# Performance work log

Hardware: AMD Instinct MI355X
Metric: run time of the kernel (lower is better)

## Reference

```python
import jax, jax.numpy as jnp
import numpy as np

H, F, E, K = 1024, 4096, 8, 2
B, S = 2, 2048

def setup_inputs() -> dict:
    key = jax.random.key(0)
    ks = jax.random.split(key, 5)
    scale = 0.02
    return {
        "x": jax.random.normal(ks[0], (B, S, H), dtype=jnp.float32),
        "router_w": jax.random.normal(ks[1], (H, E), dtype=jnp.float32) * scale,
        "router_b": jnp.zeros((E,), dtype=jnp.float32),
        "w1": jax.random.normal(ks[2], (E, H, F), dtype=jnp.float32) * scale,
        "b1": jnp.zeros((E, F), dtype=jnp.float32),
        "w2": jax.random.normal(ks[3], (E, F, H), dtype=jnp.float32) * scale,
        "b2": jnp.zeros((E, H), dtype=jnp.float32),
        "k": K,
    }

def reference(x, router_w, router_b, w1, b1, w2, b2, k):
    # Router: softmax over experts, then top-k
    scores = jnp.einsum('bsh,he->bse', x, router_w) + router_b          # [B,S,E]
    probs = jax.nn.softmax(scores, axis=-1)
    p, expert_id = jax.lax.top_k(probs, k)                               # [B,S,k]
    # Dense all-expert MLP (math identical to per-expert gather/scatter)
    h = jax.nn.gelu(jnp.einsum('bsh,ehf->bsef', x, w1) + b1,
                    approximate=False)                                    # [B,S,E,F]
    out_all = jnp.einsum('bsef,efh->bseh', h, w2) + b2                    # [B,S,E,H]
    # Gather the k selected experts per token
    out = jnp.take_along_axis(out_all, expert_id[..., None], axis=2)     # [B,S,k,H]
    # Normalize top-k probs and combine
    p = p / jnp.sum(p, axis=-1, keepdims=True)                            # [B,S,k]
    return jnp.sum(p[..., None] * out, axis=2)                            # [B,S,H]
```

## Files before the change

kernel.cpp:

```cpp
#include <hip/hip_runtime.h>
#include <hip/hip_bf16.h>
#include <math.h>

#define H 1024
#define F 4096
#define E 8
#define NTOK 4096
#define CAP 4096
#define NPAIR 8192

typedef unsigned short u16;
typedef __bf16 bf16x8 __attribute__((ext_vector_type(8)));
typedef float f32x4 __attribute__((ext_vector_type(4)));
typedef u16 u16x8 __attribute__((ext_vector_type(8)));
typedef u16 u16x4 __attribute__((ext_vector_type(4)));

__device__ inline u16 f2bf(float f) {
    union { float f; unsigned u; } v; v.f = f;
    unsigned r = v.u + 0x7fffu + ((v.u >> 16) & 1u);
    return (u16)(r >> 16);
}

__device__ inline void gload_lds16(const void* g, void* l) {
    __builtin_amdgcn_global_load_lds(
        (const __attribute__((address_space(1))) unsigned*)g,
        (__attribute__((address_space(3))) unsigned*)l, 16, 0, 0);
}

__global__ void cvt_x(const float* __restrict__ x, u16* __restrict__ xb, int n8) {
    int j = blockIdx.x * blockDim.x + threadIdx.x;
    if (j >= n8) return;
    const float4* p = (const float4*)(x + (size_t)j * 8);
    float4 a = p[0], b = p[1];
    u16x8 o;
    o[0] = f2bf(a.x); o[1] = f2bf(a.y); o[2] = f2bf(a.z); o[3] = f2bf(a.w);
    o[4] = f2bf(b.x); o[5] = f2bf(b.y); o[6] = f2bf(b.z); o[7] = f2bf(b.w);
    *(u16x8*)(xb + (size_t)j * 8) = o;
}

__global__ void transpose_cvt(const float* __restrict__ in, u16* __restrict__ out,
                              int R, int C) {
    const float* ip = in + (size_t)blockIdx.z * R * C;
    u16* op = out + (size_t)blockIdx.z * R * C;
    __shared__ float tile[64][65];
    int r0 = blockIdx.y * 64, c0 = blockIdx.x * 64;
    int tid = threadIdx.x;
    int rr = tid >> 4;
    int cc4 = (tid & 15) * 4;
    #pragma unroll
    for (int it = 0; it < 4; ++it) {
        int r = rr + it * 16;
        float4 v = *(const float4*)&ip[(size_t)(r0 + r) * C + c0 + cc4];
        tile[r][cc4 + 0] = v.x; tile[r][cc4 + 1] = v.y;
        tile[r][cc4 + 2] = v.z; tile[r][cc4 + 3] = v.w;
    }
    __syncthreads();
    int co = tid >> 3;
    int ro8 = (tid & 7) * 8;
    #pragma unroll
    for (int it = 0; it < 2; ++it) {
        int c = co + it * 32;
        u16x8 o;
        #pragma unroll
        for (int u = 0; u < 8; ++u) o[u] = f2bf(tile[ro8 + u][c]);
        *(u16x8*)&op[(size_t)(c0 + c) * R + r0 + ro8] = o;
    }
}

__global__ void router_kernel(const float* __restrict__ x, const float* __restrict__ rw,
                              const float* __restrict__ rb, int* __restrict__ counts,
                              int* __restrict__ tok_e, float* __restrict__ wgt_e) {
    int tok = blockIdx.x;
    int lane = threadIdx.x;
    float s[E] = {0.f,0.f,0.f,0.f,0.f,0.f,0.f,0.f};
    for (int r = 0; r < 4; ++r) {
        int h = r * 256 + lane * 4;
        float4 xv = *(const float4*)&x[(size_t)tok * H + h];
        const float* xf = (const float*)&xv;
        #pragma unroll
        for (int u = 0; u < 4; ++u) {
            float xs = xf[u];
            const float4* row = (const float4*)&rw[(size_t)(h + u) * E];
            float4 a = row[0], b = row[1];
            s[0] += xs * a.x; s[1] += xs * a.y; s[2] += xs * a.z; s[3] += xs * a.w;
            s[4] += xs * b.x; s[5] += xs * b.y; s[6] += xs * b.z; s[7] += xs * b.w;
        }
    }
    #pragma unroll
    for (int off = 32; off > 0; off >>= 1)
        #pragma unroll
        for (int e2 = 0; e2 < E; ++e2) s[e2] += __shfl_down(s[e2], off);
    if (lane == 0) {
        #pragma unroll
        for (int e2 = 0; e2 < E; ++e2) s[e2] += rb[e2];
        int i0 = 0;
        #pragma unroll
        for (int e2 = 1; e2 < E; ++e2) if (s[e2] > s[i0]) i0 = e2;
        int i1 = (i0 == 0) ? 1 : 0;
        #pragma unroll
        for (int e2 = 0; e2 < E; ++e2) if (e2 != i0 && s[e2] > s[i1]) i1 = e2;
        float p0 = 1.0f / (1.0f + expf(s[i1] - s[i0]));
        float p1 = 1.0f - p0;
        int pos0 = atomicAdd(&counts[i0], 1);
        tok_e[i0 * CAP + pos0] = tok; wgt_e[i0 * CAP + pos0] = p0;
        int pos1 = atomicAdd(&counts[i1], 1);
        tok_e[i1 * CAP + pos1] = tok; wgt_e[i1 * CAP + pos1] = p1;
    }
}

__global__ void scan_kernel(const int* __restrict__ counts, int* __restrict__ offsets) {
    if (threadIdx.x == 0 && blockIdx.x == 0) {
        int acc = 0;
        for (int e2 = 0; e2 < E; ++e2) { offsets[e2] = acc; acc += counts[e2]; }
    }
}

#define BM 128
#define BN 128
#define BK 32

__global__ void gemm1_kernel(const u16* __restrict__ xb, const u16* __restrict__ w1t,
                             const float* __restrict__ b1,
                             const int* __restrict__ counts, const int* __restrict__ offsets,
                             const int* __restrict__ tok_e, u16* __restrict__ hbuf) {
    int e = blockIdx.z;
    int rows = counts[e];
    int m0 = blockIdx.y * BM;
    if (m0 >= rows) return;
    int n0 = blockIdx.x * BN;
    int off = offsets[e];
    const u16* wB = w1t + (size_t)e * F * H;

    __shared__ u16 As[BM * BK];
    __shared__ u16 Bs[BN * BK];

    int tid = threadIdx.x, lane = tid & 63, w = tid >> 6;
    int wr = w >> 1, wc = w & 1;

    int i0 = w * 2, i1 = w * 2 + 1;
    int rA0 = i0 * 16 + (lane >> 2), rA1 = i1 * 16 + (lane >> 2);
    int cB = (lane & 3) * 8;
    int ia0 = m0 + rA0; if (ia0 >= rows) ia0 = rows - 1;
    int ia1 = m0 + rA1; if (ia1 >= rows) ia1 = rows - 1;
    const u16* aS0 = xb + (size_t)tok_e[e * CAP + ia0] * H + cB;
    const u16* aS1 = xb + (size_t)tok_e[e * CAP + ia1] * H + cB;
    const u16* bS0 = wB + (size_t)(n0 + rA0) * H + cB;
    const u16* bS1 = wB + (size_t)(n0 + rA1) * H + cB;
    u16* lA0 = As + i0 * 512;  u16* lA1 = As + i1 * 512;
    u16* lB0 = Bs + i0 * 512;  u16* lB1 = Bs + i1 * 512;

    int fr = lane & 15, fk = (lane >> 4) * 8;
    const u16* pa = As + (wr * 64 + fr) * BK + fk;
    const u16* pb = Bs + (wc * 64 + fr) * BK + fk;

    f32x4 acc[4][4] = {};

    for (int k0 = 0; k0 < H; k0 += BK) {
        __syncthreads();
        gload_lds16(aS0 + k0, lA0);
        gload_lds16(aS1 + k0, lA1);
        gload_lds16(bS0 + k0, lB0);
        gload_lds16(bS1 + k0, lB1);
        __syncthreads();
        bf16x8 af[4], bfr[4];
        #pragma unroll
        for (int m = 0; m < 4; ++m) af[m] = *(const bf16x8*)(pa + m * 16 * BK);
        #pragma unroll
        for (int n = 0; n < 4; ++n) bfr[n] = *(const bf16x8*)(pb + n * 16 * BK);
        #pragma unroll
        for (int m = 0; m < 4; ++m)
            #pragma unroll
            for (int n = 0; n < 4; ++n)
                acc[m][n] = __builtin_amdgcn_mfma_f32_16x16x32_bf16(bfr[n], af[m], acc[m][n], 0, 0, 0);
    }

    const float* b1e = b1 + (size_t)e * F;
    int c4 = (lane >> 4) * 4;
    #pragma unroll
    for (int m = 0; m < 4; ++m) {
        int r = m0 + wr * 64 + m * 16 + fr;
        if (r < rows) {
            u16* hrow = hbuf + (size_t)(off + r) * F;
            #pragma unroll
            for (int n = 0; n < 4; ++n) {
                int gc = n0 + wc * 64 + n * 16 + c4;
                float4 bv = *(const float4*)&b1e[gc];
                const float* bvf = (const float*)&bv;
                u16x4 ov;
                #pragma unroll
                for (int j = 0; j < 4; ++j) {
                    float v = acc[m][n][j] + bvf[j];
                    float g = 0.5f * v * (1.0f + erff(v * 0.70710678118654752f));
                    ov[j] = f2bf(g);
                }
                *(u16x4*)&hrow[gc] = ov;
            }
        }
    }
}

__global__ void gemm2_kernel(const u16* __restrict__ hbuf, const u16* __restrict__ w2t,
                             const float* __restrict__ b2,
                             const int* __restrict__ counts, const int* __restrict__ offsets,
                             const int* __restrict__ tok_e, const float* __restrict__ wgt_e,
                             float* __restrict__ out) {
    int e = blockIdx.z;
    int rows = counts[e];
    int m0 = blockIdx.y * BM;
    if (m0 >= rows) return;
    int n0 = blockIdx.x * BN;
    int off = offsets[e];
    const u16* wB = w2t + (size_t)e * H * F;

    __shared__ u16 As[BM * BK];
    __shared__ u16 Bs[BN * BK];

    int tid = threadIdx.x, lane = tid & 63, w = tid >> 6;
    int wr = w >> 1, wc = w & 1;

    int i0 = w * 2, i1 = w * 2 + 1;
    int rA0 = i0 * 16 + (lane >> 2), rA1 = i1 * 16 + (lane >> 2);
    int cB = (lane & 3) * 8;
    int ia0 = m0 + rA0; if (ia0 >= rows) ia0 = rows - 1;
    int ia1 = m0 + rA1; if (ia1 >= rows) ia1 = rows - 1;
    const u16* aS0 = hbuf + (size_t)(off + ia0) * F + cB;
    const u16* aS1 = hbuf + (size_t)(off + ia1) * F + cB;
    const u16* bS0 = wB + (size_t)(n0 + rA0) * F + cB;
    const u16* bS1 = wB + (size_t)(n0 + rA1) * F + cB;
    u16* lA0 = As + i0 * 512;  u16* lA1 = As + i1 * 512;
    u16* lB0 = Bs + i0 * 512;  u16* lB1 = Bs + i1 * 512;

    int fr = lane & 15, fk = (lane >> 4) * 8;
    const u16* pa = As + (wr * 64 + fr) * BK + fk;
    const u16* pb = Bs + (wc * 64 + fr) * BK + fk;

    f32x4 acc[4][4] = {};

    for (int k0 = 0; k0 < F; k0 += BK) {
        __syncthreads();
        gload_lds16(aS0 + k0, lA0);
        gload_lds16(aS1 + k0, lA1);
        gload_lds16(bS0 + k0, lB0);
        gload_lds16(bS1 + k0, lB1);
        __syncthreads();
        bf16x8 af[4], bfr[4];
        #pragma unroll
        for (int m = 0; m < 4; ++m) af[m] = *(const bf16x8*)(pa + m * 16 * BK);
        #pragma unroll
        for (int n = 0; n < 4; ++n) bfr[n] = *(const bf16x8*)(pb + n * 16 * BK);
        #pragma unroll
        for (int m = 0; m < 4; ++m)
            #pragma unroll
            for (int n = 0; n < 4; ++n)
                acc[m][n] = __builtin_amdgcn_mfma_f32_16x16x32_bf16(bfr[n], af[m], acc[m][n], 0, 0, 0);
    }

    const float* b2e = b2 + (size_t)e * H;
    int c4 = (lane >> 4) * 4;
    #pragma unroll
    for (int m = 0; m < 4; ++m) {
        int r = m0 + wr * 64 + m * 16 + fr;
        if (r < rows) {
            int tok = tok_e[e * CAP + r];
            float wgt = wgt_e[e * CAP + r];
            float* orow = out + (size_t)tok * H;
            #pragma unroll
            for (int n = 0; n < 4; ++n) {
                int gc = n0 + wc * 64 + n * 16 + c4;
                float4 bv = *(const float4*)&b2e[gc];
                const float* bvf = (const float*)&bv;
                #pragma unroll
                for (int j = 0; j < 4; ++j)
                    atomicAdd(&orow[gc + j], (acc[m][n][j] + bvf[j]) * wgt);
            }
        }
    }
}

extern "C" void kernel_launch(void* const* d_in, const int* in_sizes, int n_in,
                              void* d_out, int out_size, void* d_ws, size_t ws_size,
                              hipStream_t stream) {
    const float* x  = (const float*)d_in[0];
    const float* rw = (const float*)d_in[1];
    const float* rb = (const float*)d_in[2];
    const float* w1 = (const float*)d_in[3];
    const float* b1 = (const float*)d_in[4];
    const float* w2 = (const float*)d_in[5];
    const float* b2 = (const float*)d_in[6];
    float* out = (float*)d_out;

    char* ws = (char*)d_ws;
    size_t o = 0;
    u16* xb   = (u16*)(ws + o); o += (size_t)NTOK * H * 2;
    u16* w1t  = (u16*)(ws + o); o += (size_t)E * F * H * 2;
    u16* w2t  = (u16*)(ws + o); o += (size_t)E * H * F * 2;
    u16* hbuf = (u16*)(ws + o); o += (size_t)NPAIR * F * 2;
    int*   tok_e = (int*)(ws + o);   o += (size_t)E * CAP * 4;
    float* wgt_e = (float*)(ws + o); o += (size_t)E * CAP * 4;
    int*   counts  = (int*)(ws + o); o += E * 4;
    int*   offsets = (int*)(ws + o); o += E * 4;

    hipMemsetAsync(counts, 0, 2 * E * sizeof(int), stream);
    hipMemsetAsync(out, 0, (size_t)out_size * sizeof(float), stream);

    cvt_x<<<(NTOK * H / 8 + 255) / 256, 256, 0, stream>>>(x, xb, NTOK * H / 8);
    transpose_cvt<<<dim3(F / 64, H / 64, E), 256, 0, stream>>>(w1, w1t, H, F);
    transpose_cvt<<<dim3(H / 64, F / 64, E), 256, 0, stream>>>(w2, w2t, F, H);
    router_kernel<<<NTOK, 64, 0, stream>>>(x, rw, rb, counts, tok_e, wgt_e);
    scan_kernel<<<1, 64, 0, stream>>>(counts, offsets);
    gemm1_kernel<<<dim3(F / BN, CAP / BM, E), 256, 0, stream>>>(xb, w1t, b1, counts, offsets, tok_e, hbuf);
    gemm2_kernel<<<dim3(H / BN, CAP / BM, E), 256, 0, stream>>>(hbuf, w2t, b2, counts, offsets, tok_e, wgt_e, out);
}
```

Baseline: 776.2 us.

## Triple-buffer GEMM LDS loads and replace atomic scatter with a combine kernel

Both expert GEMMs now use a three-stage LDS ring with async global-to-LDS loads issued two tiles ahead and a single barrier per k-step gated by vmcnt. This hides global load latency behind MFMA work and drops one barrier per iteration. GEMM2 no longer does float atomicAdd scatter into the output. It writes per-pair results to a dense fp32 buffer, and a new combine kernel gathers each token's two rows, adds the bias and applies the weights. The cost is an extra 32MB buffer written and read back, plus one more launch, in exchange for removing the atomics and the output memset.

```diff
diff --git a/kernel.cpp b/kernel.cpp
--- a/kernel.cpp
+++ b/kernel.cpp
@@ -69,7 +69,8 @@
 
 __global__ void router_kernel(const float* __restrict__ x, const float* __restrict__ rw,
                               const float* __restrict__ rb, int* __restrict__ counts,
-                              int* __restrict__ tok_e, float* __restrict__ wgt_e) {
+                              int* __restrict__ tok_e,
+                              int* __restrict__ pair_id, float* __restrict__ pair_w) {
     int tok = blockIdx.x;
     int lane = threadIdx.x;
     float s[E] = {0.f,0.f,0.f,0.f,0.f,0.f,0.f,0.f};
@@ -102,9 +103,11 @@
         float p0 = 1.0f / (1.0f + expf(s[i1] - s[i0]));
         float p1 = 1.0f - p0;
         int pos0 = atomicAdd(&counts[i0], 1);
-        tok_e[i0 * CAP + pos0] = tok; wgt_e[i0 * CAP + pos0] = p0;
+        tok_e[i0 * CAP + pos0] = tok;
         int pos1 = atomicAdd(&counts[i1], 1);
-        tok_e[i1 * CAP + pos1] = tok; wgt_e[i1 * CAP + pos1] = p1;
+        tok_e[i1 * CAP + pos1] = tok;
+        pair_id[tok * 2]     = i0 * CAP + pos0;  pair_w[tok * 2]     = p0;
+        pair_id[tok * 2 + 1] = i1 * CAP + pos1;  pair_w[tok * 2 + 1] = p1;
     }
 }
 
@@ -118,11 +121,13 @@
 #define BM 128
 #define BN 128
 #define BK 32
-
-__global__ void gemm1_kernel(const u16* __restrict__ xb, const u16* __restrict__ w1t,
-                             const float* __restrict__ b1,
-                             const int* __restrict__ counts, const int* __restrict__ offsets,
-                             const int* __restrict__ tok_e, u16* __restrict__ hbuf) {
+#define NBUF 3
+
+__global__ __launch_bounds__(256, 3)
+void gemm1_kernel(const u16* __restrict__ xb, const u16* __restrict__ w1t,
+                  const float* __restrict__ b1,
+                  const int* __restrict__ counts, const int* __restrict__ offsets,
+                  const int* __restrict__ tok_e, u16* __restrict__ hbuf) {
     int e = blockIdx.z;
     int rows = counts[e];
     int m0 = blockIdx.y * BM;
@@ -131,13 +136,13 @@
     int off = offsets[e];
     const u16* wB = w1t + (size_t)e * F * H;
 
-    __shared__ u16 As[BM * BK];
-    __shared__ u16 Bs[BN * BK];
+    __shared__ u16 As[NBUF][BM * BK];
+    __shared__ u16 Bs[NBUF][BN * BK];
 
     int tid = threadIdx.x, lane = tid & 63, w = tid >> 6;
     int wr = w >> 1, wc = w & 1;
 
-    int i0 = w * 2, i1 = w * 2 + 1;
+    int i0 = w * 2, i1 = i0 + 1;
     int rA0 = i0 * 16 + (lane >> 2), rA1 = i1 * 16 + (lane >> 2);
     int cB = (lane & 3) * 8;
     int ia0 = m0 + rA0; if (ia0 >= rows) ia0 = rows - 1;
@@ -146,27 +151,53 @@
     const u16* aS1 = xb + (size_t)tok_e[e * CAP + ia1] * H + cB;
     const u16* bS0 = wB + (size_t)(n0 + rA0) * H + cB;
     const u16* bS1 = wB + (size_t)(n0 + rA1) * H + cB;
-    u16* lA0 = As + i0 * 512;  u16* lA1 = As + i1 * 512;
-    u16* lB0 = Bs + i0 * 512;  u16* lB1 = Bs + i1 * 512;
+    int lc0 = i0 * 512, lc1 = i1 * 512;
 
     int fr = lane & 15, fk = (lane >> 4) * 8;
-    const u16* pa = As + (wr * 64 + fr) * BK + fk;
-    const u16* pb = Bs + (wc * 64 + fr) * BK + fk;
+    int aoff = (wr * 64 + fr) * BK + fk;
+    int boff = (wc * 64 + fr) * BK + fk;
 
     f32x4 acc[4][4] = {};
-
-    for (int k0 = 0; k0 < H; k0 += BK) {
-        __syncthreads();
-        gload_lds16(aS0 + k0, lA0);
-        gload_lds16(aS1 + k0, lA1);
-        gload_lds16(bS0 + k0, lB0);
-        gload_lds16(bS1 + k0, lB1);
-        __syncthreads();
+    const int NT = H / BK;
+
+    #define STAGE1(t, b) do { int kk = (t) * BK;                 \
+        gload_lds16(aS0 + kk, &As[b][lc0]);                      \
+        gload_lds16(aS1 + kk, &As[b][lc1]);                      \
+        gload_lds16(bS0 + kk, &Bs[b][lc0]);                      \
+        gload_lds16(bS1 + kk, &Bs[b][lc1]); } while (0)
+
+    STAGE1(0, 0);
+    STAGE1(1, 1);
+    int b = 0;
+    for (int t = 0; t < NT - 1; ++t) {
+        asm volatile("s_waitcnt vmcnt(4)" ::: "memory");
+        __builtin_amdgcn_s_barrier();
+        __builtin_amdgcn_sched_barrier(0);
+        if (t + 2 < NT) {
+            int bn = b + 2; if (bn >= NBUF) bn -= NBUF;
+            STAGE1(t + 2, bn);
+        }
         bf16x8 af[4], bfr[4];
         #pragma unroll
-        for (int m = 0; m < 4; ++m) af[m] = *(const bf16x8*)(pa + m * 16 * BK);
-        #pragma unroll
-        for (int n = 0; n < 4; ++n) bfr[n] = *(const bf16x8*)(pb + n * 16 * BK);
+        for (int m = 0; m < 4; ++m) af[m] = *(const bf16x8*)&As[b][aoff + m * 16 * BK];
+        #pragma unroll
+        for (int n = 0; n < 4; ++n) bfr[n] = *(const bf16x8*)&Bs[b][boff + n * 16 * BK];
+        #pragma unroll
+        for (int m = 0; m < 4; ++m)
+            #pragma unroll
+            for (int n = 0; n < 4; ++n)
+                acc[m][n] = __builtin_amdgcn_mfma_f32_16x16x32_bf16(bfr[n], af[m], acc[m][n], 0, 0, 0);
+        ++b; if (b >= NBUF) b -= NBUF;
+    }
+    asm volatile("s_waitcnt vmcnt(0)" ::: "memory");
+    __builtin_amdgcn_s_barrier();
+    __builtin_amdgcn_sched_barrier(0);
+    {
+        bf16x8 af[4], bfr[4];
+        #pragma unroll
+        for (int m = 0; m < 4; ++m) af[m] = *(const bf16x8*)&As[b][aoff + m * 16 * BK];
+        #pragma unroll
+        for (int n = 0; n < 4; ++n) bfr[n] = *(const bf16x8*)&Bs[b][boff + n * 16 * BK];
         #pragma unroll
         for (int m = 0; m < 4; ++m)
             #pragma unroll
@@ -199,11 +230,10 @@
     }
 }
 
-__global__ void gemm2_kernel(const u16* __restrict__ hbuf, const u16* __restrict__ w2t,
-                             const float* __restrict__ b2,
-                             const int* __restrict__ counts, const int* __restrict__ offsets,
-                             const int* __restrict__ tok_e, const float* __restrict__ wgt_e,
-                             float* __restrict__ out) {
+__global__ __launch_bounds__(256, 3)
+void gemm2_kernel(const u16* __restrict__ hbuf, const u16* __restrict__ w2t,
+                  const int* __restrict__ counts, const int* __restrict__ offsets,
+                  float* __restrict__ obuf) {
     int e = blockIdx.z;
     int rows = counts[e];
     int m0 = blockIdx.y * BM;
@@ -212,13 +242,13 @@
     int off = offsets[e];
     const u16* wB = w2t + (size_t)e * H * F;
 
-    __shared__ u16 As[BM * BK];
-    __shared__ u16 Bs[BN * BK];
+    __shared__ u16 As[NBUF][BM * BK];
+    __shared__ u16 Bs[NBUF][BN * BK];
 
     int tid = threadIdx.x, lane = tid & 63, w = tid >> 6;
     int wr = w >> 1, wc = w & 1;
 
-    int i0 = w * 2, i1 = w * 2 + 1;
+    int i0 = w * 2, i1 = i0 + 1;
     int rA0 = i0 * 16 + (lane >> 2), rA1 = i1 * 16 + (lane >> 2);
     int cB = (lane & 3) * 8;
     int ia0 = m0 + rA0; if (ia0 >= rows) ia0 = rows - 1;
@@ -227,54 +257,95 @@
     const u16* aS1 = hbuf + (size_t)(off + ia1) * F + cB;
     const u16* bS0 = wB + (size_t)(n0 + rA0) * F + cB;
     const u16* bS1 = wB + (size_t)(n0 + rA1) * F + cB;
-    u16* lA0 = As + i0 * 512;  u16* lA1 = As + i1 * 512;
-    u16* lB0 = Bs + i0 * 512;  u16* lB1 = Bs + i1 * 512;
+    int lc0 = i0 * 512, lc1 = i1 * 512;
 
     int fr = lane & 15, fk = (lane >> 4) * 8;
-    const u16* pa = As + (wr * 64 + fr) * BK + fk;
-    const u16* pb = Bs + (wc * 64 + fr) * BK + fk;
+    int aoff = (wr * 64 + fr) * BK + fk;
+    int boff = (wc * 64 + fr) * BK + fk;
 
     f32x4 acc[4][4] = {};
-
-    for (int k0 = 0; k0 < F; k0 += BK) {
-        __syncthreads();
-        gload_lds16(aS0 + k0, lA0);
-        gload_lds16(aS1 + k0, lA1);
-        gload_lds16(bS0 + k0, lB0);
-        gload_lds16(bS1 + k0, lB1);
-        __syncthreads();
+    const int NT = F / BK;
+
+    #define STAGE2(t, b) do { int kk = (t) * BK;                 \
+        gload_lds16(aS0 + kk, &As[b][lc0]);                      \
+        gload_lds16(aS1 + kk, &As[b][lc1]);                      \
+        gload_lds16(bS0 + kk, &Bs[b][lc0]);                      \
+        gload_lds16(bS1 + kk, &Bs[b][lc1]); } while (0)
+
+    STAGE2(0, 0);
+    STAGE2(1, 1);
+    int b = 0;
+    for (int t = 0; t < NT - 1; ++t) {
+        asm volatile("s_waitcnt vmcnt(4)" ::: "memory");
+        __builtin_amdgcn_s_barrier();
+        __builtin_amdgcn_sched_barrier(0);
+        if (t + 2 < NT) {
+            int bn = b + 2; if (bn >= NBUF) bn -= NBUF;
+            STAGE2(t + 2, bn);
+        }
         bf16x8 af[4], bfr[4];
         #pragma unroll
-        for (int m = 0; m < 4; ++m) af[m] = *(const bf16x8*)(pa + m * 16 * BK);
-        #pragma unroll
-        for (int n = 0; n < 4; ++n) bfr[n] = *(const bf16x8*)(pb + n * 16 * BK);
+        for (int m = 0; m < 4; ++m) af[m] = *(const bf16x8*)&As[b][aoff + m * 16 * BK];
+        #pragma unroll
+        for (int n = 0; n < 4; ++n) bfr[n] = *(const bf16x8*)&Bs[b][boff + n * 16 * BK];
         #pragma unroll
         for (int m = 0; m < 4; ++m)
             #pragma unroll
             for (int n = 0; n < 4; ++n)
                 acc[m][n] = __builtin_amdgcn_mfma_f32_16x16x32_bf16(bfr[n], af[m], acc[m][n], 0, 0, 0);
-    }
-
-    const float* b2e = b2 + (size_t)e * H;
+        ++b; if (b >= NBUF) b -= NBUF;
+    }
+    asm volatile("s_waitcnt vmcnt(0)" ::: "memory");
+    __builtin_amdgcn_s_barrier();
+    __builtin_amdgcn_sched_barrier(0);
+    {
+        bf16x8 af[4], bfr[4];
+        #pragma unroll
+        for (int m = 0; m < 4; ++m) af[m] = *(const bf16x8*)&As[b][aoff + m * 16 * BK];
+        #pragma unroll
+        for (int n = 0; n < 4; ++n) bfr[n] = *(const bf16x8*)&Bs[b][boff + n * 16 * BK];
+        #pragma unroll
+        for (int m = 0; m < 4; ++m)
+            #pragma unroll
+            for (int n = 0; n < 4; ++n)
+                acc[m][n] = __builtin_amdgcn_mfma_f32_16x16x32_bf16(bfr[n], af[m], acc[m][n], 0, 0, 0);
+    }
+
     int c4 = (lane >> 4) * 4;
     #pragma unroll
     for (int m = 0; m < 4; ++m) {
         int r = m0 + wr * 64 + m * 16 + fr;
         if (r < rows) {
-            int tok = tok_e[e * CAP + r];
-            float wgt = wgt_e[e * CAP + r];
-            float* orow = out + (size_t)tok * H;
+            float* orow = obuf + (size_t)(off + r) * H;
             #pragma unroll
             for (int n = 0; n < 4; ++n) {
                 int gc = n0 + wc * 64 + n * 16 + c4;
-                float4 bv = *(const float4*)&b2e[gc];
-                const float* bvf = (const float*)&bv;
-                #pragma unroll
-                for (int j = 0; j < 4; ++j)
-                    atomicAdd(&orow[gc + j], (acc[m][n][j] + bvf[j]) * wgt);
+                *(f32x4*)&orow[gc] = acc[m][n];
             }
         }
     }
+}
+
+__global__ void combine_kernel(const float* __restrict__ obuf, const float* __restrict__ b2,
+                               const int* __restrict__ offsets,
+                               const int* __restrict__ pair_id, const float* __restrict__ pair_w,
+                               float* __restrict__ out) {
+    int tok = blockIdx.x;
+    int c4 = threadIdx.x * 4;
+    int p0 = pair_id[tok * 2], p1 = pair_id[tok * 2 + 1];
+    float w0 = pair_w[tok * 2], w1 = pair_w[tok * 2 + 1];
+    int e0 = p0 >> 12, e1 = p1 >> 12;
+    int r0 = offsets[e0] + (p0 & (CAP - 1));
+    int r1 = offsets[e1] + (p1 & (CAP - 1));
+    f32x4 a  = *(const f32x4*)&obuf[(size_t)r0 * H + c4];
+    f32x4 bb = *(const f32x4*)&obuf[(size_t)r1 * H + c4];
+    f32x4 ba0 = *(const f32x4*)&b2[(size_t)e0 * H + c4];
+    f32x4 ba1 = *(const f32x4*)&b2[(size_t)e1 * H + c4];
+    f32x4 r;
+    #pragma unroll
+    for (int j = 0; j < 4; ++j)
+        r[j] = w0 * (a[j] + ba0[j]) + w1 * (bb[j] + ba1[j]);
+    *(f32x4*)&out[(size_t)tok * H + c4] = r;
 }
 
 extern "C" void kernel_launch(void* const* d_in, const int* in_sizes, int n_in,
@@ -295,19 +366,21 @@
     u16* w1t  = (u16*)(ws + o); o += (size_t)E * F * H * 2;
     u16* w2t  = (u16*)(ws + o); o += (size_t)E * H * F * 2;
     u16* hbuf = (u16*)(ws + o); o += (size_t)NPAIR * F * 2;
-    int*   tok_e = (int*)(ws + o);   o += (size_t)E * CAP * 4;
-    float* wgt_e = (float*)(ws + o); o += (size_t)E * CAP * 4;
+    float* obuf = (float*)(ws + o); o += (size_t)NPAIR * H * 4;
+    int*   tok_e   = (int*)(ws + o); o += (size_t)E * CAP * 4;
+    int*   pair_id = (int*)(ws + o); o += (size_t)NTOK * 2 * 4;
+    float* pair_w  = (float*)(ws + o); o += (size_t)NTOK * 2 * 4;
     int*   counts  = (int*)(ws + o); o += E * 4;
     int*   offsets = (int*)(ws + o); o += E * 4;
 
     hipMemsetAsync(counts, 0, 2 * E * sizeof(int), stream);
-    hipMemsetAsync(out, 0, (size_t)out_size * sizeof(float), stream);
 
     cvt_x<<<(NTOK * H / 8 + 255) / 256, 256, 0, stream>>>(x, xb, NTOK * H / 8);
     transpose_cvt<<<dim3(F / 64, H / 64, E), 256, 0, stream>>>(w1, w1t, H, F);
     transpose_cvt<<<dim3(H / 64, F / 64, E), 256, 0, stream>>>(w2, w2t, F, H);
-    router_kernel<<<NTOK, 64, 0, stream>>>(x, rw, rb, counts, tok_e, wgt_e);
+    router_kernel<<<NTOK, 64, 0, stream>>>(x, rw, rb, counts, tok_e, pair_id, pair_w);
     scan_kernel<<<1, 64, 0, stream>>>(counts, offsets);
     gemm1_kernel<<<dim3(F / BN, CAP / BM, E), 256, 0, stream>>>(xb, w1t, b1, counts, offsets, tok_e, hbuf);
-    gemm2_kernel<<<dim3(H / BN, CAP / BM, E), 256, 0, stream>>>(hbuf, w2t, b2, counts, offsets, tok_e, wgt_e, out);
-}
+    gemm2_kernel<<<dim3(H / BN, CAP / BM, E), 256, 0, stream>>>(hbuf, w2t, counts, offsets, obuf);
+    combine_kernel<<<NTOK, 256, 0, stream>>>(obuf, b2, offsets, pair_id, pair_w, out);
+}
```

New measurement: 699.0 us. 1.11x faster.
